# Kernel optimization log

Hardware: AMD Instinct MI355X
Metric: run time of the kernel (lower is better)

## Reference

```python
import jax, jax.numpy as jnp
import numpy as np
from jax import lax

N_SRC = 2
K_BASES = 8
N_ITER = 5
NMF_EPS = 1e-20
IP_EPS = 1e-20


def setup_inputs() -> dict:
    key = jax.random.key(0)
    kx, kt, kv = jax.random.split(key, 3)
    M, J, I = 2, 2048, 1025
    X = jax.random.normal(kx, (M, J, I, 2), dtype=jnp.float32)
    T0 = jax.random.uniform(kt, (I, K_BASES, N_SRC), dtype=jnp.float32,
                            minval=1e-08, maxval=1.0)
    V0 = jax.random.uniform(kv, (K_BASES, J, N_SRC), dtype=jnp.float32,
                            minval=1e-08, maxval=1.0)
    return {"X": X, "T0": T0, "V0": V0}


def _nmf_update(Tn, Vn, Yn, eps):
    # Tn: (I,K), Vn: (K,J), Yn: (I,J) complex
    Rn = Tn @ Vn
    magR = jnp.abs(Rn)
    YdR = jnp.abs(Yn) ** 2 / (magR ** 2 + eps)   # |Y|^2 / R^2
    Rd = 1.0 / (magR + eps)
    Tn = Tn * jnp.sqrt((YdR @ Vn.T) / (Rd @ Vn.T + eps))
    Rn = Tn @ Vn
    Rd2 = 1.0 / (jnp.abs(Rn) + eps)
    Vn = Vn * jnp.sqrt((Tn.T @ YdR) / (Tn.T @ Rd2 + eps))
    return Tn, Vn, Tn @ Vn


def _ilrma(X, T0, V0):
    M, J, I, _ = X.shape
    N = N_SRC
    # view_as_complex(X.permute(2,0,1,3)) -> (I, M, J) complex
    Xc = (X[..., 0] + 1j * X[..., 1]).astype(jnp.complex64).transpose(2, 0, 1)
    eye_M = jnp.eye(M, dtype=jnp.complex64)
    W0 = jnp.broadcast_to(jnp.eye(N, M, dtype=jnp.complex64), (I, N, M))
    Y0 = jnp.einsum('inm,imj->inj', W0, Xc)

    def one_iter(carry, _):
        W, T, V, Y = carry
        for n in range(N):  # N=2, structurally distinct small loop
            Tn, Vn, Rn = _nmf_update(T[:, :, n], V[:, :, n], Y[:, n, :], NMF_EPS)
            T = T.at[:, :, n].set(Tn)
            V = V.at[:, :, n].set(Vn)
            # batched per-frequency-bin IP update (vectorizes torch's loop over i)
            inv_Rn = 1.0 / (Rn + IP_EPS)                      # (I,J)
            Xw = Xc * jnp.sqrt(inv_Rn)[:, None, :]            # (I,M,J)
            D = jnp.einsum('imj,ikj->imk', Xw, Xw.conj()) / J  # (I,M,M)
            Dreg = D + IP_EPS * eye_M
            A = jnp.einsum('inm,imk->ink', W, Dreg)           # (I,N,M), N==M
            e_n = eye_M[:, n]                                  # (M,)
            b = jnp.linalg.solve(A, jnp.broadcast_to(e_n, (I, M))[..., None])[..., 0]  # (I,M)
            Db = jnp.einsum('imk,ik->im', Dreg, b)
            denom = jnp.sqrt(jnp.real(jnp.einsum('im,im->i', b.conj(), Db)) + IP_EPS)
            W = W.at[:, n, :].set((b / denom[:, None]).conj())
        Y = jnp.einsum('inm,imj->inj', W, Xc)
        return (W, T, V, Y), None

    (W, T, V, Y), _ = lax.scan(one_iter, (W0, T0, V0, Y0), None, length=N_ITER)
    out = Y.transpose(1, 2, 0)                 # (N, J, I)
    return jnp.stack([out.real, out.imag], axis=-1)  # view_as_real -> (N,J,I,2)


def reference(X, T0, V0):
    return _ilrma(X, T0, V0)
```

## Files before the change

kernel.cpp:

```cpp
#include <hip/hip_runtime.h>

#define I_DIM 1025
#define J_DIM 2048
#define K_B 8
#define IC 33
#define EPSF 1e-20f


__device__ __forceinline__ int rev4i(int x) {
  return ((x & 1) << 3) | ((x & 2) << 1) | ((x & 4) >> 1) | ((x & 8) >> 3);
}
__device__ __forceinline__ int rev3i(int x) {
  return ((x & 1) << 2) | (x & 2) | ((x & 4) >> 2);
}

__device__ __forceinline__ void foldReduce16(float* vals, int lane) {
  #pragma unroll
  for (int step = 0; step < 4; ++step) {
    const int nv = 8 >> step;
    const int bit = (lane >> step) & 1;
    #pragma unroll
    for (int q = 0; q < nv; ++q) {
      float a = vals[q], b = vals[q + nv];
      float send = bit ? a : b;
      float keep = bit ? b : a;
      vals[q] = keep + __shfl_xor(send, 1 << step);
    }
  }
  vals[0] += __shfl_xor(vals[0], 16);
  vals[0] += __shfl_xor(vals[0], 32);
}

__device__ __forceinline__ void foldReduce8(float* vals, int lane) {
  #pragma unroll
  for (int step = 0; step < 3; ++step) {
    const int nv = 4 >> step;
    const int bit = (lane >> step) & 1;
    #pragma unroll
    for (int q = 0; q < nv; ++q) {
      float a = vals[q], b = vals[q + nv];
      float send = bit ? a : b;
      float keep = bit ? b : a;
      vals[q] = keep + __shfl_xor(send, 1 << step);
    }
  }
  vals[0] += __shfl_xor(vals[0], 8);
  vals[0] += __shfl_xor(vals[0], 16);
  vals[0] += __shfl_xor(vals[0], 32);
}

__device__ __forceinline__ float2 cmul(float2 a, float2 b) {
  return make_float2(a.x*b.x - a.y*b.y, a.x*b.y + a.y*b.x);
}
__device__ __forceinline__ float2 cadd(float2 a, float2 b) {
  return make_float2(a.x + b.x, a.y + b.y);
}
__device__ __forceinline__ float2 csub(float2 a, float2 b) {
  return make_float2(a.x - b.x, a.y - b.y);
}
__device__ __forceinline__ float2 cdiv(float2 a, float2 b) {
  float s = 1.0f / (b.x*b.x + b.y*b.y);
  return make_float2((a.x*b.x + a.y*b.y)*s, (a.y*b.x - a.x*b.y)*s);
}

__global__ __launch_bounds__(256) void k_tr_init(
    const float* __restrict__ X, float4* __restrict__ Xq,
    const float* __restrict__ T0, const float* __restrict__ V0,
    float* __restrict__ T, float* __restrict__ V, float* __restrict__ W)
{
  const int tx = threadIdx.x, ty = threadIdx.y;
  const int lt = ty * 32 + tx;
  const int bid = blockIdx.y * 33 + blockIdx.x;
  int t = bid * 256 + lt;
  if (t < 2 * K_B * J_DIM) {
    int n = t >> 14;
    int r = t & 16383;
    int p = r >> 13;
    int r2 = r & 8191;
    int j = r2 >> 2, c = r2 & 3;
    int k = p * 4 + c;
    V[t] = V0[(k * J_DIM + j) * 2 + n];
  }
  if (t < 2 * I_DIM * K_B) {
    int n = t / (I_DIM * K_B);
    int r = t % (I_DIM * K_B);
    int i = r / K_B, k = r % K_B;
    T[t] = T0[(i * K_B + k) * 2 + n];
  }
  if (t < I_DIM * 8) {
    int u = t & 7;
    int c = u & 1, m = (u >> 1) & 1, n = u >> 2;
    W[t] = (n == m && c == 0) ? 1.0f : 0.0f;
  }
  __shared__ float t0r[32][33], t0i[32][33], t1r[32][33], t1i[32][33];
  const int i0 = blockIdx.x * 32, j0 = blockIdx.y * 32;
  const float2* __restrict__ X2 = (const float2*)X;
  #pragma unroll
  for (int jj = 0; jj < 4; ++jj) {
    int jl = ty + jj * 8;
    int i = i0 + tx;
    if (i < I_DIM) {
      float2 v0 = X2[(size_t)(0 * J_DIM + j0 + jl) * I_DIM + i];
      float2 v1 = X2[(size_t)(1 * J_DIM + j0 + jl) * I_DIM + i];
      t0r[jl][tx] = v0.x; t0i[jl][tx] = v0.y;
      t1r[jl][tx] = v1.x; t1i[jl][tx] = v1.y;
    }
  }
  __syncthreads();
  #pragma unroll
  for (int ii = 0; ii < 4; ++ii) {
    int il = ty + ii * 8;
    int i = i0 + il;
    if (i < I_DIM) {
      Xq[(size_t)i * J_DIM + j0 + tx] =
        make_float4(t0r[tx][il], t0i[tx][il], t1r[tx][il], t1i[tx][il]);
    }
  }
}

template<int N>
__device__ __forceinline__ void nmfT_src(
    int i, int tid,
    const float4* __restrict__ Xq, float* __restrict__ T,
    const float4* __restrict__ V4, const float* __restrict__ W,
    float* __restrict__ YdR)
{
  float4 xs[8];
  #pragma unroll
  for (int u = 0; u < 8; ++u) xs[u] = Xq[(size_t)i * J_DIM + u * 256 + tid];

  const float4 w = ((const float4*)W)[i * 2 + N];
  const int trow = (N * I_DIM + i) * K_B;
  float t[K_B];
  #pragma unroll
  for (int k = 0; k < K_B; ++k) t[k] = T[trow + k];

  float num[K_B], den[K_B];
  #pragma unroll
  for (int k = 0; k < K_B; ++k) { num[k] = 0.f; den[k] = 0.f; }

  #pragma unroll
  for (int u = 0; u < 8; ++u) {
    int j = u * 256 + tid;
    float4 va = V4[(N * 2 + 0) * J_DIM + j];
    float4 vb = V4[(N * 2 + 1) * J_DIM + j];
    float v[K_B] = {va.x, va.y, va.z, va.w, vb.x, vb.y, vb.z, vb.w};
    float rn = 0.f;
    #pragma unroll
    for (int k = 0; k < K_B; ++k) rn += t[k] * v[k];
    float4 x = xs[u];
    float yr = w.x * x.x - w.y * x.y + w.z * x.z - w.w * x.w;
    float yi = w.x * x.y + w.y * x.x + w.z * x.w + w.w * x.z;
    float rd = __builtin_amdgcn_rcpf(fabsf(rn) + EPSF);
    float ydr = (yr * yr + yi * yi) * rd * rd;
    YdR[(size_t)i * J_DIM + j] = ydr;
    #pragma unroll
    for (int k = 0; k < K_B; ++k) { num[k] += ydr * v[k]; den[k] += rd * v[k]; }
  }

  float vals[16];
  #pragma unroll
  for (int k = 0; k < K_B; ++k) { vals[k] = num[k]; vals[K_B + k] = den[k]; }
  const int wave = tid >> 6, lane = tid & 63;
  foldReduce16(vals, lane);
  __shared__ float redT[4][16];
  if (lane < 16) redT[wave][lane] = vals[0];
  __syncthreads();
  if (tid < K_B) {
    int r = rev4i(tid);
    float nm = redT[0][r] + redT[1][r] + redT[2][r] + redT[3][r];
    float dn = redT[0][r+1] + redT[1][r+1] + redT[2][r+1] + redT[3][r+1];
    T[trow + tid] *= sqrtf(nm / (dn + EPSF));
  }
}

__device__ __forceinline__ void ip_solve_both(
    int i,
    float D000, float p0, float q0, float D110,
    float D001, float p1, float q1, float D111,
    float* __restrict__ W)
{
  float4 w0 = ((const float4*)W)[i * 2 + 0];
  float4 w1 = ((const float4*)W)[i * 2 + 1];
  float2 W00 = make_float2(w0.x, w0.y), W01 = make_float2(w0.z, w0.w);
  float2 W10 = make_float2(w1.x, w1.y), W11 = make_float2(w1.z, w1.w);
  {
    float D00 = D000 + EPSF, D11 = D110 + EPSF;
    float2 D01 = make_float2(p0, q0);
    float2 D10 = make_float2(p0, -q0);
    float2 A00 = cadd(make_float2(W00.x * D00, W00.y * D00), cmul(W01, D10));
    float2 A01 = cadd(cmul(W00, D01), make_float2(W01.x * D11, W01.y * D11));
    float2 A10 = cadd(make_float2(W10.x * D00, W10.y * D00), cmul(W11, D10));
    float2 A11 = cadd(cmul(W10, D01), make_float2(W11.x * D11, W11.y * D11));
    float2 det = csub(cmul(A00, A11), cmul(A01, A10));
    float2 b0 = cdiv(A11, det);
    float2 b1 = cdiv(make_float2(-A10.x, -A10.y), det);
    float2 Db0 = cadd(make_float2(D00 * b0.x, D00 * b0.y), cmul(D01, b1));
    float2 Db1 = cadd(cmul(D10, b0), make_float2(D11 * b1.x, D11 * b1.y));
    float ip = b0.x * Db0.x + b0.y * Db0.y + b1.x * Db1.x + b1.y * Db1.y;
    float inv = 1.0f / sqrtf(ip + EPSF);
    W00 = make_float2(b0.x * inv, -b0.y * inv);
    W01 = make_float2(b1.x * inv, -b1.y * inv);
  }
  {
    float D00 = D001 + EPSF, D11 = D111 + EPSF;
    float2 D01 = make_float2(p1, q1);
    float2 D10 = make_float2(p1, -q1);
    float2 A00 = cadd(make_float2(W00.x * D00, W00.y * D00), cmul(W01, D10));
    float2 A01 = cadd(cmul(W00, D01), make_float2(W01.x * D11, W01.y * D11));
    float2 A10 = cadd(make_float2(W10.x * D00, W10.y * D00), cmul(W11, D10));
    float2 A11 = cadd(cmul(W10, D01), make_float2(W11.x * D11, W11.y * D11));
    float2 det = csub(cmul(A00, A11), cmul(A01, A10));
    float2 b0 = cdiv(make_float2(-A01.x, -A01.y), det);
    float2 b1 = cdiv(A00, det);
    float2 Db0 = cadd(make_float2(D00 * b0.x, D00 * b0.y), cmul(D01, b1));
    float2 Db1 = cadd(cmul(D10, b0), make_float2(D11 * b1.x, D11 * b1.y));
    float ip = b0.x * Db0.x + b0.y * Db0.y + b1.x * Db1.x + b1.y * Db1.y;
    float inv = 1.0f / sqrtf(ip + EPSF);
    W10 = make_float2(b0.x * inv, -b0.y * inv);
    W11 = make_float2(b1.x * inv, -b1.y * inv);
  }
  ((float4*)W)[i * 2 + 0] = make_float4(W00.x, W00.y, W01.x, W01.y);
  ((float4*)W)[i * 2 + 1] = make_float4(W10.x, W10.y, W11.x, W11.y);
}

__global__ __launch_bounds__(256) void k_nmf2(
    const float4* __restrict__ Xq, float* __restrict__ T,
    const float4* __restrict__ V4, const float* __restrict__ W,
    float* __restrict__ Y0, float* __restrict__ Y1)
{
  int b = blockIdx.x;
  int p, pop;
  if (b >= 2048) { p = 1024; pop = b - 2048; }
  else { pop = (b >> 3) & 1; p = ((b >> 4) << 3) | (b & 7); }
  if (pop == 0)
    nmfT_src<0>(p, threadIdx.x, Xq, T, V4, W, Y0);
  else
    nmfT_src<1>(p, threadIdx.x, Xq, T, V4, W, Y1);
}

__global__ __launch_bounds__(256) void k_part2(
    const float* __restrict__ T, const float4* __restrict__ V4,
    const float* __restrict__ Y0, const float* __restrict__ Y1,
    float4* __restrict__ Pn0, float4* __restrict__ Pd0,
    float4* __restrict__ Pn1, float4* __restrict__ Pd1)
{
  const int vb = blockIdx.x;
  const int tid = threadIdx.x;
  const int src = vb / 264;
  const int pb = vb % 264;
  const int jb = pb & 7, c = pb >> 3;
  const int i0 = c * 32;
  const int ni = min(32, I_DIM - i0);
  __shared__ float4 sT4[64];
  if (tid < ni * 2)
    sT4[tid] = ((const float4*)(T + (size_t)(src * I_DIM + i0) * K_B))[tid];
  __syncthreads();

  const float* __restrict__ YdR = src ? Y1 : Y0;
  float4* __restrict__ Pn = src ? Pn1 : Pn0;
  float4* __restrict__ Pd = src ? Pd1 : Pd0;
  const int j = jb * 256 + tid;
  float4 va = V4[(src * 2 + 0) * J_DIM + j];
  float4 vb4 = V4[(src * 2 + 1) * J_DIM + j];
  float v[K_B] = {va.x, va.y, va.z, va.w, vb4.x, vb4.y, vb4.z, vb4.w};
  float num[K_B], den[K_B];
  #pragma unroll
  for (int k = 0; k < K_B; ++k) { num[k] = 0.f; den[k] = 0.f; }

  if (ni == 32) {
    #pragma unroll
    for (int g = 0; g < 4; ++g) {
      float yd[8];
      #pragma unroll
      for (int q = 0; q < 8; ++q)
        yd[q] = YdR[(size_t)(i0 + g * 8 + q) * J_DIM + j];
      #pragma unroll
      for (int q = 0; q < 8; ++q) {
        const int ii = g * 8 + q;
        float4 ta = sT4[ii * 2], tb = sT4[ii * 2 + 1];
        float tk[K_B] = {ta.x, ta.y, ta.z, ta.w, tb.x, tb.y, tb.z, tb.w};
        float rn = 0.f;
        #pragma unroll
        for (int k = 0; k < K_B; ++k) rn += tk[k] * v[k];
        float rd2 = __builtin_amdgcn_rcpf(fabsf(rn) + EPSF);
        #pragma unroll
        for (int k = 0; k < K_B; ++k) {
          num[k] += tk[k] * yd[q];
          den[k] += tk[k] * rd2;
        }
      }
    }
  } else {
    for (int ii = 0; ii < ni; ++ii) {
      float ydr = YdR[(size_t)(i0 + ii) * J_DIM + j];
      float4 ta = sT4[ii * 2], tb = sT4[ii * 2 + 1];
      float tk[K_B] = {ta.x, ta.y, ta.z, ta.w, tb.x, tb.y, tb.z, tb.w};
      float rn = 0.f;
      #pragma unroll
      for (int k = 0; k < K_B; ++k) rn += tk[k] * v[k];
      float rd2 = __builtin_amdgcn_rcpf(fabsf(rn) + EPSF);
      #pragma unroll
      for (int k = 0; k < K_B; ++k) {
        num[k] += tk[k] * ydr;
        den[k] += tk[k] * rd2;
      }
    }
  }
  Pn[((size_t)c * 2 + 0) * J_DIM + j] = make_float4(num[0], num[1], num[2], num[3]);
  Pn[((size_t)c * 2 + 1) * J_DIM + j] = make_float4(num[4], num[5], num[6], num[7]);
  Pd[((size_t)c * 2 + 0) * J_DIM + j] = make_float4(den[0], den[1], den[2], den[3]);
  Pd[((size_t)c * 2 + 1) * J_DIM + j] = make_float4(den[4], den[5], den[6], den[7]);
}

__global__ __launch_bounds__(256) void k_fin2(
    float4* __restrict__ V4,
    const float4* __restrict__ Pn0, const float4* __restrict__ Pd0,
    const float4* __restrict__ Pn1, const float4* __restrict__ Pd1)
{
  const int vb = blockIdx.x;
  const int tid = threadIdx.x;
  const int src = vb >> 4, fb = vb & 15;
  const float4* __restrict__ Pn = src ? Pn1 : Pn0;
  const float4* __restrict__ Pd = src ? Pd1 : Pd0;
  const int t4 = fb * 256 + tid;
  float4 nm = make_float4(0.f, 0.f, 0.f, 0.f);
  float4 dn = make_float4(0.f, 0.f, 0.f, 0.f);
  #pragma unroll
  for (int c = 0; c < IC; ++c) {
    float4 a = Pn[(size_t)c * 4096 + t4];
    float4 bb = Pd[(size_t)c * 4096 + t4];
    nm.x += a.x; nm.y += a.y; nm.z += a.z; nm.w += a.w;
    dn.x += bb.x; dn.y += bb.y; dn.z += bb.z; dn.w += bb.w;
  }
  float4 v = V4[src * 4096 + t4];
  v.x *= sqrtf(nm.x / (dn.x + EPSF));
  v.y *= sqrtf(nm.y / (dn.y + EPSF));
  v.z *= sqrtf(nm.z / (dn.z + EPSF));
  v.w *= sqrtf(nm.w / (dn.w + EPSF));
  V4[src * 4096 + t4] = v;
}

__global__ __launch_bounds__(256) void k_ip2(
    const float4* __restrict__ Xq, const float* __restrict__ T,
    const float4* __restrict__ V4, float* __restrict__ W)
{
  const int i = blockIdx.x;
  const int tid = threadIdx.x;
  float4 xs[8];
  #pragma unroll
  for (int u = 0; u < 8; ++u) xs[u] = Xq[(size_t)i * J_DIM + u * 256 + tid];

  float t0[K_B], t1[K_B];
  #pragma unroll
  for (int k = 0; k < K_B; ++k) {
    t0[k] = T[(0 * I_DIM + i) * K_B + k];
    t1[k] = T[(1 * I_DIM + i) * K_B + k];
  }
  float acc[8];
  #pragma unroll
  for (int q = 0; q < 8; ++q) acc[q] = 0.f;

  #pragma unroll
  for (int u = 0; u < 8; ++u) {
    int j = u * 256 + tid;
    float4 va0 = V4[0 * J_DIM + j];
    float4 vb0 = V4[1 * J_DIM + j];
    float4 va1 = V4[2 * J_DIM + j];
    float4 vb1 = V4[3 * J_DIM + j];
    float rn0 = t0[0]*va0.x + t0[1]*va0.y + t0[2]*va0.z + t0[3]*va0.w
              + t0[4]*vb0.x + t0[5]*vb0.y + t0[6]*vb0.z + t0[7]*vb0.w;
    float rn1 = t1[0]*va1.x + t1[1]*va1.y + t1[2]*va1.z + t1[3]*va1.w
              + t1[4]*vb1.x + t1[5]*vb1.y + t1[6]*vb1.z + t1[7]*vb1.w;
    float w0 = __builtin_amdgcn_rcpf(rn0 + EPSF);
    float w1 = __builtin_amdgcn_rcpf(rn1 + EPSF);
    float4 x = xs[u];
    float m00 = x.x * x.x + x.y * x.y;
    float m11 = x.z * x.z + x.w * x.w;
    float m01r = x.x * x.z + x.y * x.w;
    float m01i = x.y * x.z - x.x * x.w;
    acc[0] += m00 * w0; acc[1] += m01r * w0; acc[2] += m01i * w0; acc[3] += m11 * w0;
    acc[4] += m00 * w1; acc[5] += m01r * w1; acc[6] += m01i * w1; acc[7] += m11 * w1;
  }
  const int wave = tid >> 6, lane = tid & 63;
  foldReduce8(acc, lane);
  __shared__ float redI[4][8];
  if (lane < 8) redI[wave][lane] = acc[0];
  __syncthreads();
  if (tid == 0) {
    const float invJ = 1.0f / (float)J_DIM;
    float s[8];
    #pragma unroll
    for (int vv = 0; vv < 8; ++vv) {
      int r = rev3i(vv);
      s[vv] = (redI[0][r] + redI[1][r] + redI[2][r] + redI[3][r]) * invJ;
    }
    ip_solve_both(i, s[0], s[1], s[2], s[3], s[4], s[5], s[6], s[7], W);
  }
}

__global__ __launch_bounds__(256) void k_out(
    const float* __restrict__ X, const float* __restrict__ W, float* __restrict__ out)
{
  const int j = blockIdx.x;
  const int i = blockIdx.y * 256 + threadIdx.x;
  if (i >= I_DIM) return;
  const float2* __restrict__ X2 = (const float2*)X;
  float2 x0 = X2[(size_t)(0 * J_DIM + j) * I_DIM + i];
  float2 x1 = X2[(size_t)(1 * J_DIM + j) * I_DIM + i];
  const float4* __restrict__ W4 = (const float4*)W;
  float4 w0 = W4[i * 2 + 0];
  float4 w1 = W4[i * 2 + 1];
  float2* __restrict__ O = (float2*)out;
  float yr = w0.x * x0.x - w0.y * x0.y + w0.z * x1.x - w0.w * x1.y;
  float yi = w0.x * x0.y + w0.y * x0.x + w0.z * x1.y + w0.w * x1.x;
  O[(size_t)(0 * J_DIM + j) * I_DIM + i] = make_float2(yr, yi);
  yr = w1.x * x0.x - w1.y * x0.y + w1.z * x1.x - w1.w * x1.y;
  yi = w1.x * x0.y + w1.y * x0.x + w1.z * x1.y + w1.w * x1.x;
  O[(size_t)(1 * J_DIM + j) * I_DIM + i] = make_float2(yr, yi);
}

extern "C" void kernel_launch(void* const* d_in, const int* in_sizes, int n_in,
                              void* d_out, int out_size, void* d_ws, size_t ws_size,
                              hipStream_t stream) {
  const float* X  = (const float*)d_in[0];
  const float* T0 = (const float*)d_in[1];
  const float* V0 = (const float*)d_in[2];
  float* ws = (float*)d_ws;
  float4* Xq  = (float4*)ws;
  float* Y0   = ws + 8396800;
  float* Y1   = ws + 10496000;
  float* T    = ws + 12595200;
  float* V    = ws + 12611600;
  float* W    = ws + 12644368;
  float4* Pn0 = (float4*)(ws + 12652568);
  float4* Pd0 = (float4*)(ws + 13193240);
  float4* Pn1 = (float4*)(ws + 13733912);
  float4* Pd1 = (float4*)(ws + 14274584);
  float4* V4  = (float4*)V;
  float* outp = (float*)d_out;

  k_tr_init<<<dim3(33, 64), dim3(32, 8), 0, stream>>>(X, Xq, T0, V0, T, V, W);
  for (int it = 0; it < 5; ++it) {
    k_nmf2<<<2 * I_DIM, 256, 0, stream>>>(Xq, T, V4, W, Y0, Y1);
    k_part2<<<528, 256, 0, stream>>>(T, V4, Y0, Y1, Pn0, Pd0, Pn1, Pd1);
    k_fin2<<<32, 256, 0, stream>>>(V4, Pn0, Pd0, Pn1, Pd1);
    k_ip2<<<I_DIM, 256, 0, stream>>>(Xq, T, V4, W);
  }
  k_out<<<dim3(J_DIM, 5), 256, 0, stream>>>(X, W, outp);
}
```

Before: 276.8 us.

## Store YdR intermediate as bf16, batch V loads, trim k_out grid

The |Y|^2/R^2 intermediate passed from k_nmf2 to k_part2 is now stored as bf16 instead of fp32, halving that buffer's write and read traffic. The T-update sums use the rounded value so both kernels see consistent data. V loads in k_nmf2 and k_ip2 are grouped four at a time to raise memory-level parallelism. k_out's grid shrinks from 5 to 4 row blocks, with the final frequency bin handled by one extra thread per block. The bf16 storage loses precision in an iterative NMF update, which could push results outside tolerance.

```diff
diff --git a/kernel.cpp b/kernel.cpp
--- a/kernel.cpp
+++ b/kernel.cpp
@@ -12,6 +12,15 @@
 }
 __device__ __forceinline__ int rev3i(int x) {
   return ((x & 1) << 2) | (x & 2) | ((x & 4) >> 2);
+}
+
+__device__ __forceinline__ unsigned short f2bf(float f) {
+  unsigned u = __float_as_uint(f);
+  unsigned r = (u + 0x7FFFu + ((u >> 16) & 1u)) >> 16;
+  return (unsigned short)r;
+}
+__device__ __forceinline__ float bf2f(unsigned short h) {
+  return __uint_as_float(((unsigned)h) << 16);
 }
 
 __device__ __forceinline__ void foldReduce16(float* vals, int lane) {
@@ -123,7 +132,7 @@
     int i, int tid,
     const float4* __restrict__ Xq, float* __restrict__ T,
     const float4* __restrict__ V4, const float* __restrict__ W,
-    float* __restrict__ YdR)
+    unsigned short* __restrict__ YdR)
 {
   float4 xs[8];
   #pragma unroll
@@ -140,22 +149,33 @@
   for (int k = 0; k < K_B; ++k) { num[k] = 0.f; den[k] = 0.f; }
 
   #pragma unroll
-  for (int u = 0; u < 8; ++u) {
-    int j = u * 256 + tid;
-    float4 va = V4[(N * 2 + 0) * J_DIM + j];
-    float4 vb = V4[(N * 2 + 1) * J_DIM + j];
-    float v[K_B] = {va.x, va.y, va.z, va.w, vb.x, vb.y, vb.z, vb.w};
-    float rn = 0.f;
-    #pragma unroll
-    for (int k = 0; k < K_B; ++k) rn += t[k] * v[k];
-    float4 x = xs[u];
-    float yr = w.x * x.x - w.y * x.y + w.z * x.z - w.w * x.w;
-    float yi = w.x * x.y + w.y * x.x + w.z * x.w + w.w * x.z;
-    float rd = __builtin_amdgcn_rcpf(fabsf(rn) + EPSF);
-    float ydr = (yr * yr + yi * yi) * rd * rd;
-    YdR[(size_t)i * J_DIM + j] = ydr;
-    #pragma unroll
-    for (int k = 0; k < K_B; ++k) { num[k] += ydr * v[k]; den[k] += rd * v[k]; }
+  for (int h = 0; h < 2; ++h) {
+    float4 va[4], vb[4];
+    #pragma unroll
+    for (int q = 0; q < 4; ++q) {
+      int j = (h * 4 + q) * 256 + tid;
+      va[q] = V4[(N * 2 + 0) * J_DIM + j];
+      vb[q] = V4[(N * 2 + 1) * J_DIM + j];
+    }
+    #pragma unroll
+    for (int q = 0; q < 4; ++q) {
+      int u = h * 4 + q;
+      int j = u * 256 + tid;
+      float v[K_B] = {va[q].x, va[q].y, va[q].z, va[q].w,
+                      vb[q].x, vb[q].y, vb[q].z, vb[q].w};
+      float rn = 0.f;
+      #pragma unroll
+      for (int k = 0; k < K_B; ++k) rn += t[k] * v[k];
+      float4 x = xs[u];
+      float yr = w.x * x.x - w.y * x.y + w.z * x.z - w.w * x.w;
+      float yi = w.x * x.y + w.y * x.x + w.z * x.w + w.w * x.z;
+      float rd = __builtin_amdgcn_rcpf(fabsf(rn) + EPSF);
+      float ydr = (yr * yr + yi * yi) * rd * rd;
+      YdR[(size_t)i * J_DIM + j] = f2bf(ydr);
+      float ydq = bf2f(f2bf(ydr));
+      #pragma unroll
+      for (int k = 0; k < K_B; ++k) { num[k] += ydq * v[k]; den[k] += rd * v[k]; }
+    }
   }
 
   float vals[16];
@@ -227,7 +247,7 @@
 __global__ __launch_bounds__(256) void k_nmf2(
     const float4* __restrict__ Xq, float* __restrict__ T,
     const float4* __restrict__ V4, const float* __restrict__ W,
-    float* __restrict__ Y0, float* __restrict__ Y1)
+    unsigned short* __restrict__ Y0, unsigned short* __restrict__ Y1)
 {
   int b = blockIdx.x;
   int p, pop;
@@ -241,7 +261,7 @@
 
 __global__ __launch_bounds__(256) void k_part2(
     const float* __restrict__ T, const float4* __restrict__ V4,
-    const float* __restrict__ Y0, const float* __restrict__ Y1,
+    const unsigned short* __restrict__ Y0, const unsigned short* __restrict__ Y1,
     float4* __restrict__ Pn0, float4* __restrict__ Pd0,
     float4* __restrict__ Pn1, float4* __restrict__ Pd1)
 {
@@ -257,7 +277,7 @@
     sT4[tid] = ((const float4*)(T + (size_t)(src * I_DIM + i0) * K_B))[tid];
   __syncthreads();
 
-  const float* __restrict__ YdR = src ? Y1 : Y0;
+  const unsigned short* __restrict__ YdR = src ? Y1 : Y0;
   float4* __restrict__ Pn = src ? Pn1 : Pn0;
   float4* __restrict__ Pd = src ? Pd1 : Pd0;
   const int j = jb * 256 + tid;
@@ -271,13 +291,14 @@
   if (ni == 32) {
     #pragma unroll
     for (int g = 0; g < 4; ++g) {
-      float yd[8];
+      unsigned short yd[8];
       #pragma unroll
       for (int q = 0; q < 8; ++q)
         yd[q] = YdR[(size_t)(i0 + g * 8 + q) * J_DIM + j];
       #pragma unroll
       for (int q = 0; q < 8; ++q) {
         const int ii = g * 8 + q;
+        float ydr = bf2f(yd[q]);
         float4 ta = sT4[ii * 2], tb = sT4[ii * 2 + 1];
         float tk[K_B] = {ta.x, ta.y, ta.z, ta.w, tb.x, tb.y, tb.z, tb.w};
         float rn = 0.f;
@@ -286,14 +307,14 @@
         float rd2 = __builtin_amdgcn_rcpf(fabsf(rn) + EPSF);
         #pragma unroll
         for (int k = 0; k < K_B; ++k) {
-          num[k] += tk[k] * yd[q];
+          num[k] += tk[k] * ydr;
           den[k] += tk[k] * rd2;
         }
       }
     }
   } else {
     for (int ii = 0; ii < ni; ++ii) {
-      float ydr = YdR[(size_t)(i0 + ii) * J_DIM + j];
+      float ydr = bf2f(YdR[(size_t)(i0 + ii) * J_DIM + j]);
       float4 ta = sT4[ii * 2], tb = sT4[ii * 2 + 1];
       float tk[K_B] = {ta.x, ta.y, ta.z, ta.w, tb.x, tb.y, tb.z, tb.w};
       float rn = 0.f;
@@ -362,25 +383,33 @@
   for (int q = 0; q < 8; ++q) acc[q] = 0.f;
 
   #pragma unroll
-  for (int u = 0; u < 8; ++u) {
-    int j = u * 256 + tid;
-    float4 va0 = V4[0 * J_DIM + j];
-    float4 vb0 = V4[1 * J_DIM + j];
-    float4 va1 = V4[2 * J_DIM + j];
-    float4 vb1 = V4[3 * J_DIM + j];
-    float rn0 = t0[0]*va0.x + t0[1]*va0.y + t0[2]*va0.z + t0[3]*va0.w
-              + t0[4]*vb0.x + t0[5]*vb0.y + t0[6]*vb0.z + t0[7]*vb0.w;
-    float rn1 = t1[0]*va1.x + t1[1]*va1.y + t1[2]*va1.z + t1[3]*va1.w
-              + t1[4]*vb1.x + t1[5]*vb1.y + t1[6]*vb1.z + t1[7]*vb1.w;
-    float w0 = __builtin_amdgcn_rcpf(rn0 + EPSF);
-    float w1 = __builtin_amdgcn_rcpf(rn1 + EPSF);
-    float4 x = xs[u];
-    float m00 = x.x * x.x + x.y * x.y;
-    float m11 = x.z * x.z + x.w * x.w;
-    float m01r = x.x * x.z + x.y * x.w;
-    float m01i = x.y * x.z - x.x * x.w;
-    acc[0] += m00 * w0; acc[1] += m01r * w0; acc[2] += m01i * w0; acc[3] += m11 * w0;
-    acc[4] += m00 * w1; acc[5] += m01r * w1; acc[6] += m01i * w1; acc[7] += m11 * w1;
+  for (int h = 0; h < 2; ++h) {
+    float4 va0[4], vb0[4], va1[4], vb1[4];
+    #pragma unroll
+    for (int q = 0; q < 4; ++q) {
+      int j = (h * 4 + q) * 256 + tid;
+      va0[q] = V4[0 * J_DIM + j];
+      vb0[q] = V4[1 * J_DIM + j];
+      va1[q] = V4[2 * J_DIM + j];
+      vb1[q] = V4[3 * J_DIM + j];
+    }
+    #pragma unroll
+    for (int q = 0; q < 4; ++q) {
+      int u = h * 4 + q;
+      float rn0 = t0[0]*va0[q].x + t0[1]*va0[q].y + t0[2]*va0[q].z + t0[3]*va0[q].w
+                + t0[4]*vb0[q].x + t0[5]*vb0[q].y + t0[6]*vb0[q].z + t0[7]*vb0[q].w;
+      float rn1 = t1[0]*va1[q].x + t1[1]*va1[q].y + t1[2]*va1[q].z + t1[3]*va1[q].w
+                + t1[4]*vb1[q].x + t1[5]*vb1[q].y + t1[6]*vb1[q].z + t1[7]*vb1[q].w;
+      float w0 = __builtin_amdgcn_rcpf(rn0 + EPSF);
+      float w1 = __builtin_amdgcn_rcpf(rn1 + EPSF);
+      float4 x = xs[u];
+      float m00 = x.x * x.x + x.y * x.y;
+      float m11 = x.z * x.z + x.w * x.w;
+      float m01r = x.x * x.z + x.y * x.w;
+      float m01i = x.y * x.z - x.x * x.w;
+      acc[0] += m00 * w0; acc[1] += m01r * w0; acc[2] += m01i * w0; acc[3] += m11 * w0;
+      acc[4] += m00 * w1; acc[5] += m01r * w1; acc[6] += m01i * w1; acc[7] += m11 * w1;
+    }
   }
   const int wave = tid >> 6, lane = tid & 63;
   foldReduce8(acc, lane);
@@ -404,20 +433,34 @@
 {
   const int j = blockIdx.x;
   const int i = blockIdx.y * 256 + threadIdx.x;
-  if (i >= I_DIM) return;
   const float2* __restrict__ X2 = (const float2*)X;
-  float2 x0 = X2[(size_t)(0 * J_DIM + j) * I_DIM + i];
-  float2 x1 = X2[(size_t)(1 * J_DIM + j) * I_DIM + i];
   const float4* __restrict__ W4 = (const float4*)W;
-  float4 w0 = W4[i * 2 + 0];
-  float4 w1 = W4[i * 2 + 1];
   float2* __restrict__ O = (float2*)out;
-  float yr = w0.x * x0.x - w0.y * x0.y + w0.z * x1.x - w0.w * x1.y;
-  float yi = w0.x * x0.y + w0.y * x0.x + w0.z * x1.y + w0.w * x1.x;
-  O[(size_t)(0 * J_DIM + j) * I_DIM + i] = make_float2(yr, yi);
-  yr = w1.x * x0.x - w1.y * x0.y + w1.z * x1.x - w1.w * x1.y;
-  yi = w1.x * x0.y + w1.y * x0.x + w1.z * x1.y + w1.w * x1.x;
-  O[(size_t)(1 * J_DIM + j) * I_DIM + i] = make_float2(yr, yi);
+  {
+    float2 x0 = X2[(size_t)(0 * J_DIM + j) * I_DIM + i];
+    float2 x1 = X2[(size_t)(1 * J_DIM + j) * I_DIM + i];
+    float4 w0 = W4[i * 2 + 0];
+    float4 w1 = W4[i * 2 + 1];
+    float yr = w0.x * x0.x - w0.y * x0.y + w0.z * x1.x - w0.w * x1.y;
+    float yi = w0.x * x0.y + w0.y * x0.x + w0.z * x1.y + w0.w * x1.x;
+    O[(size_t)(0 * J_DIM + j) * I_DIM + i] = make_float2(yr, yi);
+    yr = w1.x * x0.x - w1.y * x0.y + w1.z * x1.x - w1.w * x1.y;
+    yi = w1.x * x0.y + w1.y * x0.x + w1.z * x1.y + w1.w * x1.x;
+    O[(size_t)(1 * J_DIM + j) * I_DIM + i] = make_float2(yr, yi);
+  }
+  if (blockIdx.y == 0 && threadIdx.x == 0) {
+    const int il = 1024;
+    float2 x0 = X2[(size_t)(0 * J_DIM + j) * I_DIM + il];
+    float2 x1 = X2[(size_t)(1 * J_DIM + j) * I_DIM + il];
+    float4 w0 = W4[il * 2 + 0];
+    float4 w1 = W4[il * 2 + 1];
+    float yr = w0.x * x0.x - w0.y * x0.y + w0.z * x1.x - w0.w * x1.y;
+    float yi = w0.x * x0.y + w0.y * x0.x + w0.z * x1.y + w0.w * x1.x;
+    O[(size_t)(0 * J_DIM + j) * I_DIM + il] = make_float2(yr, yi);
+    yr = w1.x * x0.x - w1.y * x0.y + w1.z * x1.x - w1.w * x1.y;
+    yi = w1.x * x0.y + w1.y * x0.x + w1.z * x1.y + w1.w * x1.x;
+    O[(size_t)(1 * J_DIM + j) * I_DIM + il] = make_float2(yr, yi);
+  }
 }
 
 extern "C" void kernel_launch(void* const* d_in, const int* in_sizes, int n_in,
@@ -428,8 +471,8 @@
   const float* V0 = (const float*)d_in[2];
   float* ws = (float*)d_ws;
   float4* Xq  = (float4*)ws;
-  float* Y0   = ws + 8396800;
-  float* Y1   = ws + 10496000;
+  unsigned short* Y0 = (unsigned short*)(ws + 8396800);
+  unsigned short* Y1 = (unsigned short*)(ws + 10496000);
   float* T    = ws + 12595200;
   float* V    = ws + 12611600;
   float* W    = ws + 12644368;
@@ -447,5 +490,5 @@
     k_fin2<<<32, 256, 0, stream>>>(V4, Pn0, Pd0, Pn1, Pd1);
     k_ip2<<<I_DIM, 256, 0, stream>>>(Xq, T, V4, W);
   }
-  k_out<<<dim3(J_DIM, 5), 256, 0, stream>>>(X, W, outp);
-}
+  k_out<<<dim3(J_DIM, 4), 256, 0, stream>>>(X, W, outp);
+}
```

Measured after the change: 275.1 us. No clear change (-0.6%).
